# Optimization experiments

Hardware: AMD Instinct MI355X
Metric: run time of the kernel (lower is better)

## Reference

```python
import jax, jax.numpy as jnp
import numpy as np

G, NPG, HID, NLAYERS, MAXZ, K = 256, 128, 256, 3, 1000, 30
N = G * NPG          # 32768 nodes
E = N * 16           # 524288 edges
TOTAL_DIM = HID * NLAYERS + 1  # 769


def setup_inputs():
    key = jax.random.key(0)
    ks = jax.random.split(key, 12)
    z = jax.random.randint(ks[0], (N,), 0, MAXZ)
    edge_index = jax.random.randint(ks[1], (2, E), 0, N)
    batch = jnp.arange(N) // NPG  # contiguous equal-size graphs
    emb = jax.random.normal(ks[2], (MAXZ, HID), jnp.float32)
    s = 1.0 / np.sqrt(HID)
    gcn_w = jax.random.normal(ks[3], (NLAYERS, HID, HID), jnp.float32) * s
    gcn_b = jnp.zeros((NLAYERS, HID), jnp.float32)
    gcn_w_last = jax.random.normal(ks[4], (HID, 1), jnp.float32) * s
    gcn_b_last = jnp.zeros((1,), jnp.float32)
    conv1_w = jax.random.normal(ks[5], (16, 1, 5), jnp.float32) * (1.0 / np.sqrt(5))
    conv1_b = jnp.zeros((16,), jnp.float32)
    conv2_w = jax.random.normal(ks[6], (32, 16, 5), jnp.float32) * (1.0 / np.sqrt(80))
    conv2_b = jnp.zeros((32,), jnp.float32)
    kd = K * TOTAL_DIM            # 23070
    flat = 32 * ((kd - 4) // 2 - 4)  # 368928
    lin1_w = jax.random.normal(ks[7], (128, flat), jnp.float32) * (1.0 / np.sqrt(flat))
    lin1_b = jnp.zeros((128,), jnp.float32)
    lin2_w = jax.random.normal(ks[8], (1, 128), jnp.float32) * (1.0 / np.sqrt(128))
    lin2_b = jnp.zeros((1,), jnp.float32)
    return dict(z=z, edge_index=edge_index, batch=batch, emb=emb, gcn_w=gcn_w,
                gcn_b=gcn_b, gcn_w_last=gcn_w_last, gcn_b_last=gcn_b_last,
                conv1_w=conv1_w, conv1_b=conv1_b, conv2_w=conv2_w, conv2_b=conv2_b,
                lin1_w=lin1_w, lin1_b=lin1_b, lin2_w=lin2_w, lin2_b=lin2_b)


def reference(z, edge_index, batch, emb, gcn_w, gcn_b, gcn_w_last, gcn_b_last,
              conv1_w, conv1_b, conv2_w, conv2_b, lin1_w, lin1_b, lin2_w, lin2_b):
    src, dst = edge_index[0], edge_index[1]
    # GCNConv normalization with self-loops: D^{-1/2}(A+I)D^{-1/2}
    deg = 1.0 + jax.ops.segment_sum(jnp.ones((E,), jnp.float32), dst, num_segments=N)
    dinv = jax.lax.rsqrt(deg)
    enorm = dinv[src] * dinv[dst]   # per-edge norm
    snorm = 1.0 / deg               # self-loop norm

    def gcn(x, W, b):
        xw = x @ W
        agg = jax.ops.segment_sum(enorm[:, None] * xw[src], dst, num_segments=N)
        return agg + snorm[:, None] * xw + b

    x = emb[z]
    xs = []
    for i in range(NLAYERS):
        x = jnp.tanh(gcn(x, gcn_w[i], gcn_b[i]))
        xs.append(x)
    xs.append(jnp.tanh(gcn(x, gcn_w_last, gcn_b_last)))
    h = jnp.concatenate(xs, axis=-1)  # [N, TOTAL_DIM]

    # global_sort_pool: per-graph descending sort by last channel, keep top-k
    hg = h.reshape(G, NPG, TOTAL_DIM)
    order = jnp.argsort(-hg[:, :, -1], axis=1)
    hg = jnp.take_along_axis(hg, order[:, :, None], axis=1)[:, :K]
    p = hg.reshape(G, 1, K * TOTAL_DIM)

    dn = ('NCH', 'OIH', 'NCH')
    c = jax.lax.conv_general_dilated(p, conv1_w, (1,), 'VALID', dimension_numbers=dn)
    c = jax.nn.relu(c + conv1_b[None, :, None])
    c = jax.lax.reduce_window(c, -jnp.inf, jax.lax.max, (1, 1, 2), (1, 1, 2), 'VALID')
    c = jax.lax.conv_general_dilated(c, conv2_w, (1,), 'VALID', dimension_numbers=dn)
    c = jax.nn.relu(c + conv2_b[None, :, None])
    f = c.reshape(G, -1)
    f = jax.nn.relu(f @ lin1_w.T + lin1_b)
    return (f @ lin2_w.T + lin2_b).reshape(-1)
```

## Files before the change

kernel.cpp:

```cpp
#include <hip/hip_runtime.h>

#define NN      32768
#define EE      524288
#define GG      256
#define NPG     128
#define HID     256
#define KTOP    30
#define TD      769
#define HSTR    772
#define PLEN    23070
#define C1LEN   23066
#define POOLLEN 11533
#define C2LEN   11529
#define FLAT    368928
#define L1_KRANGE 1920
#define L1_KS   193

__global__ __launch_bounds__(256) void k_deg(const int* __restrict__ dst, int* __restrict__ deg_cnt) {
    int e = blockIdx.x * 256 + threadIdx.x;
    atomicAdd(&deg_cnt[dst[e]], 1);
}

__global__ __launch_bounds__(256) void k_norm(const int* __restrict__ deg_cnt,
                                              float* __restrict__ dinv, float* __restrict__ snorm) {
    int n = blockIdx.x * 256 + threadIdx.x;
    float dg = 1.0f + (float)deg_cnt[n];
    dinv[n] = rsqrtf(dg);
    snorm[n] = 1.0f / dg;
}

__global__ __launch_bounds__(1024) void k_scan(const int* __restrict__ deg_cnt, int* __restrict__ row_start) {
    __shared__ int sA[1024];
    int t = threadIdx.x;
    int base = t * 32;
    int s = 0;
    for (int i = 0; i < 32; i++) s += deg_cnt[base + i];
    sA[t] = s;
    __syncthreads();
    for (int off = 1; off < 1024; off <<= 1) {
        int v = (t >= off) ? sA[t - off] : 0;
        __syncthreads();
        sA[t] += v;
        __syncthreads();
    }
    int run = sA[t] - s;
    for (int i = 0; i < 32; i++) { row_start[base + i] = run; run += deg_cnt[base + i]; }
}

__global__ __launch_bounds__(256) void k_csrfill(const int* __restrict__ src, const int* __restrict__ dst,
                                                 const int* __restrict__ row_start, int* __restrict__ fill,
                                                 const float* __restrict__ dinv,
                                                 int* __restrict__ csr_src, float* __restrict__ csr_w) {
    int e = blockIdx.x * 256 + threadIdx.x;
    int s = src[e], d = dst[e];
    int pos = row_start[d] + atomicAdd(&fill[d], 1);
    csr_src[pos] = s;
    csr_w[pos] = dinv[s] * dinv[d];
}

__global__ __launch_bounds__(256) void k_embed(const int* __restrict__ z, const float* __restrict__ emb,
                                               float* __restrict__ x) {
    int i = blockIdx.x * 256 + threadIdx.x;
    int n = i >> 6, l = i & 63;
    ((float4*)x)[(size_t)n * 64 + l] = ((const float4*)emb)[(size_t)z[n] * 64 + l];
}

__global__ __launch_bounds__(256) void k_gemm_gcn(const float* __restrict__ A, const float* __restrict__ B,
                                                  float* __restrict__ C) {
    __shared__ float As[16][132];
    __shared__ float Bs[16][132];
    int m0 = blockIdx.x * 128;
    int n0 = blockIdx.y * 128;
    int tid = threadIdx.x;
    int ty = tid >> 4, tx = tid & 15;
    float acc[8][8] = {};
    for (int k0 = 0; k0 < 256; k0 += 16) {
        {
            int m = tid >> 2, kq = (tid & 3) * 4;
            #pragma unroll
            for (int r = 0; r < 2; r++) {
                float4 v = *(const float4*)&A[(size_t)(m0 + m + 64 * r) * 256 + k0 + kq];
                As[kq + 0][m + 64 * r] = v.x;
                As[kq + 1][m + 64 * r] = v.y;
                As[kq + 2][m + 64 * r] = v.z;
                As[kq + 3][m + 64 * r] = v.w;
            }
            int n = (tid & 31) * 4, kk = tid >> 5;
            #pragma unroll
            for (int r = 0; r < 2; r++) {
                float4 v = *(const float4*)&B[(size_t)(k0 + kk + 8 * r) * 256 + n0 + n];
                *(float4*)&Bs[kk + 8 * r][n] = v;
            }
        }
        __syncthreads();
        #pragma unroll
        for (int k = 0; k < 16; k++) {
            float a[8], b[8];
            *(float4*)&a[0] = *(float4*)&As[k][ty * 8];
            *(float4*)&a[4] = *(float4*)&As[k][ty * 8 + 4];
            *(float4*)&b[0] = *(float4*)&Bs[k][tx * 8];
            *(float4*)&b[4] = *(float4*)&Bs[k][tx * 8 + 4];
            #pragma unroll
            for (int i = 0; i < 8; i++)
                #pragma unroll
                for (int j = 0; j < 8; j++) acc[i][j] += a[i] * b[j];
        }
        __syncthreads();
    }
    #pragma unroll
    for (int i = 0; i < 8; i++) {
        int m = m0 + ty * 8 + i;
        float4 v0 = make_float4(acc[i][0], acc[i][1], acc[i][2], acc[i][3]);
        float4 v1 = make_float4(acc[i][4], acc[i][5], acc[i][6], acc[i][7]);
        *(float4*)&C[(size_t)m * 256 + n0 + tx * 8] = v0;
        *(float4*)&C[(size_t)m * 256 + n0 + tx * 8 + 4] = v1;
    }
}

__global__ __launch_bounds__(256) void k_agg(const float* __restrict__ xw, const int* __restrict__ row_start,
                                             const int* __restrict__ deg_cnt, const int* __restrict__ csr_src,
                                             const float* __restrict__ csr_w, const float* __restrict__ snorm,
                                             const float* __restrict__ bias, float* __restrict__ xn,
                                             float* __restrict__ h, int hoff) {
    int d = blockIdx.x * 4 + (threadIdx.x >> 6);
    int l = threadIdx.x & 63;
    float4 v = ((const float4*)xw)[(size_t)d * 64 + l];
    float sn = snorm[d];
    float4 acc = make_float4(sn * v.x, sn * v.y, sn * v.z, sn * v.w);
    int st = row_start[d], cnt = deg_cnt[d];
    for (int j = 0; j < cnt; j++) {
        int s = csr_src[st + j];
        float w = csr_w[st + j];
        float4 u = ((const float4*)xw)[(size_t)s * 64 + l];
        acc.x += w * u.x; acc.y += w * u.y; acc.z += w * u.z; acc.w += w * u.w;
    }
    float4 b = ((const float4*)bias)[l];
    acc.x = tanhf(acc.x + b.x);
    acc.y = tanhf(acc.y + b.y);
    acc.z = tanhf(acc.z + b.z);
    acc.w = tanhf(acc.w + b.w);
    ((float4*)xn)[(size_t)d * 64 + l] = acc;
    *(float4*)&h[(size_t)d * HSTR + hoff + l * 4] = acc;
}

__global__ __launch_bounds__(256) void k_dot_last(const float* __restrict__ x, const float* __restrict__ wl,
                                                  float* __restrict__ xwl) {
    int d = blockIdx.x * 4 + (threadIdx.x >> 6);
    int l = threadIdx.x & 63;
    float4 v = ((const float4*)x)[(size_t)d * 64 + l];
    float4 w = ((const float4*)wl)[l];
    float s = v.x * w.x + v.y * w.y + v.z * w.z + v.w * w.w;
    #pragma unroll
    for (int off = 32; off; off >>= 1) s += __shfl_down(s, off, 64);
    if (l == 0) xwl[d] = s;
}

__global__ __launch_bounds__(256) void k_agg_last(const float* __restrict__ xwl, const int* __restrict__ row_start,
                                                  const int* __restrict__ deg_cnt, const int* __restrict__ csr_src,
                                                  const float* __restrict__ csr_w, const float* __restrict__ snorm,
                                                  const float* __restrict__ blast, float* __restrict__ h) {
    int d = blockIdx.x * 256 + threadIdx.x;
    float acc = snorm[d] * xwl[d];
    int st = row_start[d], cnt = deg_cnt[d];
    for (int j = 0; j < cnt; j++) acc += csr_w[st + j] * xwl[csr_src[st + j]];
    h[(size_t)d * HSTR + 768] = tanhf(acc + blast[0]);
}

__global__ __launch_bounds__(128) void k_sort_gather(const float* __restrict__ h, float* __restrict__ P) {
    __shared__ float kk[128];
    __shared__ int ii[128];
    int g = blockIdx.x, t = threadIdx.x;
    kk[t] = h[(size_t)(g * 128 + t) * HSTR + 768];
    ii[t] = t;
    __syncthreads();
    for (int size = 2; size <= 128; size <<= 1) {
        for (int stride = size >> 1; stride > 0; stride >>= 1) {
            int p = t ^ stride;
            if (p > t) {
                float ka = kk[t], kbv = kk[p];
                int ia = ii[t], ib = ii[p];
                bool aFirst = (ka > kbv) || (ka == kbv && ia < ib);
                bool asc = (t & size) == 0;
                if (asc != aFirst) { kk[t] = kbv; kk[p] = ka; ii[t] = ib; ii[p] = ia; }
            }
            __syncthreads();
        }
    }
    float* Pg = P + (size_t)g * PLEN;
    for (int r = 0; r < KTOP; r++) {
        const float* srcp = h + (size_t)(g * 128 + ii[r]) * HSTR;
        for (int c = t; c < TD; c += 128) Pg[(size_t)r * TD + c] = srcp[c];
    }
}

#define JT 128
__global__ __launch_bounds__(256) void k_conv(const float* __restrict__ P,
                                              const float* __restrict__ w1, const float* __restrict__ b1,
                                              const float* __restrict__ w2, const float* __restrict__ b2,
                                              float* __restrict__ f) {
    __shared__ float sl[272];
    __shared__ float pool[16][136];
    __shared__ float w2t[80][32];
    __shared__ float w1s[16][5];
    __shared__ float b1s[16];
    __shared__ float b2s[32];
    int g = blockIdx.x;
    int j0 = blockIdx.y * JT;
    int tid = threadIdx.x;
    const float* Pg = P + (size_t)g * PLEN;
    for (int i = tid; i < 268; i += 256) sl[i] = Pg[min(2 * j0 + i, PLEN - 1)];
    for (int i = tid; i < 80; i += 256) w1s[i / 5][i % 5] = w1[i];
    if (tid < 16) b1s[tid] = b1[tid];
    if (tid < 32) b2s[tid] = b2[tid];
    for (int i = tid; i < 2560; i += 256) {
        int c2 = i / 80, rem = i % 80;
        w2t[rem][c2] = w2[i];
    }
    __syncthreads();
    for (int i = tid; i < 16 * 132; i += 256) {
        int c1 = i / 132, t = i % 132;
        int u = 2 * t;
        float a = b1s[c1], b = a;
        #pragma unroll
        for (int q = 0; q < 5; q++) {
            a += w1s[c1][q] * sl[u + q];
            b += w1s[c1][q] * sl[u + 1 + q];
        }
        pool[c1][t] = fmaxf(fmaxf(a, b), 0.0f);
    }
    __syncthreads();
    int wv = tid >> 6;
    int jl = tid & 63;
    int c2o = wv * 8;
    float acc[8][2];
    #pragma unroll
    for (int cc = 0; cc < 8; cc++) {
        float bb = b2s[c2o + cc];
        acc[cc][0] = bb; acc[cc][1] = bb;
    }
    #pragma unroll 4
    for (int c1 = 0; c1 < 16; c1++) {
        #pragma unroll
        for (int k = 0; k < 5; k++) {
            float4 w0 = *(float4*)&w2t[c1 * 5 + k][c2o];
            float4 w1v = *(float4*)&w2t[c1 * 5 + k][c2o + 4];
            float p0 = pool[c1][jl + k];
            float p1 = pool[c1][jl + 64 + k];
            acc[0][0] += w0.x * p0; acc[0][1] += w0.x * p1;
            acc[1][0] += w0.y * p0; acc[1][1] += w0.y * p1;
            acc[2][0] += w0.z * p0; acc[2][1] += w0.z * p1;
            acc[3][0] += w0.w * p0; acc[3][1] += w0.w * p1;
            acc[4][0] += w1v.x * p0; acc[4][1] += w1v.x * p1;
            acc[5][0] += w1v.y * p0; acc[5][1] += w1v.y * p1;
            acc[6][0] += w1v.z * p0; acc[6][1] += w1v.z * p1;
            acc[7][0] += w1v.w * p0; acc[7][1] += w1v.w * p1;
        }
    }
    size_t fg = (size_t)g * FLAT;
    #pragma unroll
    for (int cc = 0; cc < 8; cc++) {
        #pragma unroll
        for (int jj = 0; jj < 2; jj++) {
            int j = j0 + jl + 64 * jj;
            if (j < C2LEN) f[fg + (size_t)(c2o + cc) * C2LEN + j] = fmaxf(acc[cc][jj], 0.0f);
        }
    }
}

__global__ __launch_bounds__(256) void k_lin1(const float* __restrict__ f, const float* __restrict__ W,
                                              float* __restrict__ partial) {
    __shared__ float As[32][68];
    __shared__ float Bs[32][132];
    int m0 = blockIdx.x * 64;
    int ks = blockIdx.y;
    int kbase = ks * L1_KRANGE;
    int kend = min(kbase + L1_KRANGE, FLAT);
    int tid = threadIdx.x;
    int ty = tid >> 5, tx = tid & 31;
    float acc[8][4] = {};
    for (int k0 = kbase; k0 < kend; k0 += 32) {
        {
            int m = tid >> 2, kq = (tid & 3) * 8;
            #pragma unroll
            for (int r = 0; r < 2; r++) {
                int k = kq + r * 4;
                float4 v = *(const float4*)&f[(size_t)(m0 + m) * FLAT + k0 + k];
                As[k + 0][m] = v.x; As[k + 1][m] = v.y; As[k + 2][m] = v.z; As[k + 3][m] = v.w;
            }
            int n = tid >> 3, kq2 = (tid & 7) * 4;
            #pragma unroll
            for (int r = 0; r < 4; r++) {
                int nn = n + 32 * r;
                float4 v = *(const float4*)&W[(size_t)nn * FLAT + k0 + kq2];
                Bs[kq2 + 0][nn] = v.x; Bs[kq2 + 1][nn] = v.y; Bs[kq2 + 2][nn] = v.z; Bs[kq2 + 3][nn] = v.w;
            }
        }
        __syncthreads();
        #pragma unroll
        for (int k = 0; k < 32; k++) {
            float a[8], bv[4];
            *(float4*)&a[0] = *(float4*)&As[k][ty * 8];
            *(float4*)&a[4] = *(float4*)&As[k][ty * 8 + 4];
            *(float4*)&bv[0] = *(float4*)&Bs[k][tx * 4];
            #pragma unroll
            for (int i = 0; i < 8; i++)
                #pragma unroll
                for (int j = 0; j < 4; j++) acc[i][j] += a[i] * bv[j];
        }
        __syncthreads();
    }
    #pragma unroll
    for (int i = 0; i < 8; i++) {
        int m = m0 + ty * 8 + i;
        float4 v = make_float4(acc[i][0], acc[i][1], acc[i][2], acc[i][3]);
        *(float4*)&partial[((size_t)ks * 256 + m) * 128 + tx * 4] = v;
    }
}

__global__ __launch_bounds__(128) void k_reduce(const float* __restrict__ partial, const float* __restrict__ lb1,
                                                const float* __restrict__ lw2, const float* __restrict__ lb2,
                                                float* __restrict__ out) {
    int g = blockIdx.x, o = threadIdx.x;
    float s = 0.0f;
    for (int ks = 0; ks < L1_KS; ks++) s += partial[((size_t)ks * 256 + g) * 128 + o];
    float v = fmaxf(s + lb1[o], 0.0f) * lw2[o];
    #pragma unroll
    for (int off = 32; off; off >>= 1) v += __shfl_down(v, off, 64);
    __shared__ float red[2];
    if ((threadIdx.x & 63) == 0) red[threadIdx.x >> 6] = v;
    __syncthreads();
    if (threadIdx.x == 0) out[g] = red[0] + red[1] + lb2[0];
}

extern "C" void kernel_launch(void* const* d_in, const int* in_sizes, int n_in,
                              void* d_out, int out_size, void* d_ws, size_t ws_size,
                              hipStream_t stream) {
    const int*   z     = (const int*)d_in[0];
    const int*   ei    = (const int*)d_in[1];
    const int*   srcv  = ei;
    const int*   dstv  = ei + EE;
    const float* emb   = (const float*)d_in[3];
    const float* gcnw  = (const float*)d_in[4];
    const float* gcnb  = (const float*)d_in[5];
    const float* wlast = (const float*)d_in[6];
    const float* blast = (const float*)d_in[7];
    const float* w1    = (const float*)d_in[8];
    const float* b1    = (const float*)d_in[9];
    const float* w2    = (const float*)d_in[10];
    const float* b2    = (const float*)d_in[11];
    const float* l1w   = (const float*)d_in[12];
    const float* l1b   = (const float*)d_in[13];
    const float* l2w   = (const float*)d_in[14];
    const float* l2b   = (const float*)d_in[15];
    float* out = (float*)d_out;

    char* base = (char*)d_ws;
    const size_t FB = ((size_t)GG * FLAT * 4 + 511) & ~(size_t)511;
    float* fbuf = (float*)base;
    char* p = base;
    auto alloc = [&](size_t bytes) { void* r = (void*)p; p += (bytes + 511) & ~(size_t)511; return r; };
    int*   deg_cnt = (int*)  alloc((size_t)NN * 4);
    int*   fill    = (int*)  alloc((size_t)NN * 4);
    int*   rowst   = (int*)  alloc((size_t)NN * 4);
    int*   csr_src = (int*)  alloc((size_t)EE * 4);
    float* csr_w   = (float*)alloc((size_t)EE * 4);
    float* dinv    = (float*)alloc((size_t)NN * 4);
    float* snorm   = (float*)alloc((size_t)NN * 4);
    float* xA      = (float*)alloc((size_t)NN * 256 * 4);
    float* xB      = (float*)alloc((size_t)NN * 256 * 4);
    float* xw      = (float*)alloc((size_t)NN * 256 * 4);
    float* h       = (float*)alloc((size_t)NN * HSTR * 4);
    float* xwl     = (float*)alloc((size_t)NN * 4);
    float* P       = (float*)(base + FB);
    float* partial = (float*)(base + FB + (((size_t)GG * PLEN * 4 + 511) & ~(size_t)511));
    (void)ws_size; (void)in_sizes; (void)n_in; (void)out_size;

    hipMemsetAsync(deg_cnt, 0, (size_t)NN * 4, stream);
    hipMemsetAsync(fill,    0, (size_t)NN * 4, stream);

    k_deg    <<<EE / 256, 256, 0, stream>>>(dstv, deg_cnt);
    k_norm   <<<NN / 256, 256, 0, stream>>>(deg_cnt, dinv, snorm);
    k_scan   <<<1, 1024, 0, stream>>>(deg_cnt, rowst);
    k_csrfill<<<EE / 256, 256, 0, stream>>>(srcv, dstv, rowst, fill, dinv, csr_src, csr_w);
    k_embed  <<<NN * 64 / 256, 256, 0, stream>>>(z, emb, xA);

    float* xc = xA;
    float* xn = xB;
    for (int layer = 0; layer < 3; layer++) {
        k_gemm_gcn<<<dim3(NN / 128, 2), 256, 0, stream>>>(xc, gcnw + (size_t)layer * 65536, xw);
        k_agg<<<NN / 4, 256, 0, stream>>>(xw, rowst, deg_cnt, csr_src, csr_w, snorm,
                                          gcnb + layer * 256, xn, h, layer * 256);
        float* t = xc; xc = xn; xn = t;
    }
    k_dot_last<<<NN / 4, 256, 0, stream>>>(xc, wlast, xwl);
    k_agg_last<<<NN / 256, 256, 0, stream>>>(xwl, rowst, deg_cnt, csr_src, csr_w, snorm, blast, h);

    k_sort_gather<<<GG, 128, 0, stream>>>(h, P);

    k_conv<<<dim3(GG, (C2LEN + JT - 1) / JT), 256, 0, stream>>>(P, w1, b1, w2, b2, fbuf);

    k_lin1  <<<dim3(4, L1_KS), 256, 0, stream>>>(fbuf, l1w, partial);
    k_reduce<<<GG, 128, 0, stream>>>(partial, l1b, l2w, l2b, out);
}
```

Baseline: 1.477 ms.

## Retile lin1 GEMM, fuse last-layer dot into aggregation, split conv1 input even/odd

The lin1 split-K GEMM now uses 128x128 output tiles with an 8x8 per-thread microtile, a 16-deep k step and a smaller k range per block. This halves the number of times the large lin1 weight matrix is re-read across M tiles and raises the block count along K. The separate k_dot_last kernel is folded into the third k_agg launch, which saves one pass over the node features and one launch. The conv1 input in shared memory is split into even and odd arrays, so the stride-2 pooled convolution reads consecutive addresses. The trade-off is more partial sums for k_reduce to add and higher register use in lin1.

```diff
diff --git a/kernel.cpp b/kernel.cpp
--- a/kernel.cpp
+++ b/kernel.cpp
@@ -13,8 +13,8 @@
 #define POOLLEN 11533
 #define C2LEN   11529
 #define FLAT    368928
-#define L1_KRANGE 1920
-#define L1_KS   193
+#define L1_KRANGE 1024
+#define L1_KS   361
 
 __global__ __launch_bounds__(256) void k_deg(const int* __restrict__ dst, int* __restrict__ deg_cnt) {
     int e = blockIdx.x * 256 + threadIdx.x;
@@ -121,7 +121,8 @@
                                              const int* __restrict__ deg_cnt, const int* __restrict__ csr_src,
                                              const float* __restrict__ csr_w, const float* __restrict__ snorm,
                                              const float* __restrict__ bias, float* __restrict__ xn,
-                                             float* __restrict__ h, int hoff) {
+                                             float* __restrict__ h, int hoff,
+                                             const float* __restrict__ wl, float* __restrict__ xwl) {
     int d = blockIdx.x * 4 + (threadIdx.x >> 6);
     int l = threadIdx.x & 63;
     float4 v = ((const float4*)xw)[(size_t)d * 64 + l];
@@ -141,18 +142,13 @@
     acc.w = tanhf(acc.w + b.w);
     ((float4*)xn)[(size_t)d * 64 + l] = acc;
     *(float4*)&h[(size_t)d * HSTR + hoff + l * 4] = acc;
-}
-
-__global__ __launch_bounds__(256) void k_dot_last(const float* __restrict__ x, const float* __restrict__ wl,
-                                                  float* __restrict__ xwl) {
-    int d = blockIdx.x * 4 + (threadIdx.x >> 6);
-    int l = threadIdx.x & 63;
-    float4 v = ((const float4*)x)[(size_t)d * 64 + l];
-    float4 w = ((const float4*)wl)[l];
-    float s = v.x * w.x + v.y * w.y + v.z * w.z + v.w * w.w;
-    #pragma unroll
-    for (int off = 32; off; off >>= 1) s += __shfl_down(s, off, 64);
-    if (l == 0) xwl[d] = s;
+    if (wl != nullptr) {
+        float4 w4 = ((const float4*)wl)[l];
+        float s = acc.x * w4.x + acc.y * w4.y + acc.z * w4.z + acc.w * w4.w;
+        #pragma unroll
+        for (int off = 32; off; off >>= 1) s += __shfl_down(s, off, 64);
+        if (l == 0) xwl[d] = s;
+    }
 }
 
 __global__ __launch_bounds__(256) void k_agg_last(const float* __restrict__ xwl, const int* __restrict__ row_start,
@@ -198,7 +194,8 @@
                                               const float* __restrict__ w1, const float* __restrict__ b1,
                                               const float* __restrict__ w2, const float* __restrict__ b2,
                                               float* __restrict__ f) {
-    __shared__ float sl[272];
+    __shared__ float sle[136];
+    __shared__ float slo[136];
     __shared__ float pool[16][136];
     __shared__ float w2t[80][32];
     __shared__ float w1s[16][5];
@@ -208,7 +205,10 @@
     int j0 = blockIdx.y * JT;
     int tid = threadIdx.x;
     const float* Pg = P + (size_t)g * PLEN;
-    for (int i = tid; i < 268; i += 256) sl[i] = Pg[min(2 * j0 + i, PLEN - 1)];
+    for (int i = tid; i < 268; i += 256) {
+        float v = Pg[min(2 * j0 + i, PLEN - 1)];
+        if (i & 1) slo[i >> 1] = v; else sle[i >> 1] = v;
+    }
     for (int i = tid; i < 80; i += 256) w1s[i / 5][i % 5] = w1[i];
     if (tid < 16) b1s[tid] = b1[tid];
     if (tid < 32) b2s[tid] = b2[tid];
@@ -219,13 +219,10 @@
     __syncthreads();
     for (int i = tid; i < 16 * 132; i += 256) {
         int c1 = i / 132, t = i % 132;
-        int u = 2 * t;
-        float a = b1s[c1], b = a;
-        #pragma unroll
-        for (int q = 0; q < 5; q++) {
-            a += w1s[c1][q] * sl[u + q];
-            b += w1s[c1][q] * sl[u + 1 + q];
-        }
+        float e0 = sle[t], o0 = slo[t], e1 = sle[t + 1], o1 = slo[t + 1], e2 = sle[t + 2], o2 = slo[t + 2];
+        float w0 = w1s[c1][0], w1v = w1s[c1][1], w2v = w1s[c1][2], w3 = w1s[c1][3], w4 = w1s[c1][4];
+        float a = b1s[c1] + w0 * e0 + w1v * o0 + w2v * e1 + w3 * o1 + w4 * e2;
+        float b = b1s[c1] + w0 * o0 + w1v * e1 + w2v * o1 + w3 * e2 + w4 * o2;
         pool[c1][t] = fmaxf(fmaxf(a, b), 0.0f);
     }
     __syncthreads();
@@ -269,51 +266,56 @@
 
 __global__ __launch_bounds__(256) void k_lin1(const float* __restrict__ f, const float* __restrict__ W,
                                               float* __restrict__ partial) {
-    __shared__ float As[32][68];
-    __shared__ float Bs[32][132];
-    int m0 = blockIdx.x * 64;
+    __shared__ float As[16][132];
+    __shared__ float Bs[16][132];
+    int m0 = blockIdx.x * 128;
     int ks = blockIdx.y;
     int kbase = ks * L1_KRANGE;
     int kend = min(kbase + L1_KRANGE, FLAT);
     int tid = threadIdx.x;
-    int ty = tid >> 5, tx = tid & 31;
-    float acc[8][4] = {};
-    for (int k0 = kbase; k0 < kend; k0 += 32) {
+    int ty = tid >> 4, tx = tid & 15;
+    float acc[8][8] = {};
+    for (int k0 = kbase; k0 < kend; k0 += 16) {
         {
-            int m = tid >> 2, kq = (tid & 3) * 8;
+            int m = tid >> 2, kq = (tid & 3) * 4;
             #pragma unroll
             for (int r = 0; r < 2; r++) {
-                int k = kq + r * 4;
-                float4 v = *(const float4*)&f[(size_t)(m0 + m) * FLAT + k0 + k];
-                As[k + 0][m] = v.x; As[k + 1][m] = v.y; As[k + 2][m] = v.z; As[k + 3][m] = v.w;
+                float4 v = *(const float4*)&f[(size_t)(m0 + m + 64 * r) * FLAT + k0 + kq];
+                As[kq + 0][m + 64 * r] = v.x;
+                As[kq + 1][m + 64 * r] = v.y;
+                As[kq + 2][m + 64 * r] = v.z;
+                As[kq + 3][m + 64 * r] = v.w;
             }
-            int n = tid >> 3, kq2 = (tid & 7) * 4;
-            #pragma unroll
-            for (int r = 0; r < 4; r++) {
-                int nn = n + 32 * r;
-                float4 v = *(const float4*)&W[(size_t)nn * FLAT + k0 + kq2];
-                Bs[kq2 + 0][nn] = v.x; Bs[kq2 + 1][nn] = v.y; Bs[kq2 + 2][nn] = v.z; Bs[kq2 + 3][nn] = v.w;
+            int n = tid >> 1, kq2 = (tid & 1) * 8;
+            #pragma unroll
+            for (int r = 0; r < 2; r++) {
+                int k = kq2 + r * 4;
+                float4 v = *(const float4*)&W[(size_t)n * FLAT + k0 + k];
+                Bs[k + 0][n] = v.x; Bs[k + 1][n] = v.y; Bs[k + 2][n] = v.z; Bs[k + 3][n] = v.w;
             }
         }
         __syncthreads();
         #pragma unroll
-        for (int k = 0; k < 32; k++) {
-            float a[8], bv[4];
+        for (int k = 0; k < 16; k++) {
+            float a[8], b[8];
             *(float4*)&a[0] = *(float4*)&As[k][ty * 8];
             *(float4*)&a[4] = *(float4*)&As[k][ty * 8 + 4];
-            *(float4*)&bv[0] = *(float4*)&Bs[k][tx * 4];
+            *(float4*)&b[0] = *(float4*)&Bs[k][tx * 8];
+            *(float4*)&b[4] = *(float4*)&Bs[k][tx * 8 + 4];
             #pragma unroll
             for (int i = 0; i < 8; i++)
                 #pragma unroll
-                for (int j = 0; j < 4; j++) acc[i][j] += a[i] * bv[j];
+                for (int j = 0; j < 8; j++) acc[i][j] += a[i] * b[j];
         }
         __syncthreads();
     }
     #pragma unroll
     for (int i = 0; i < 8; i++) {
         int m = m0 + ty * 8 + i;
-        float4 v = make_float4(acc[i][0], acc[i][1], acc[i][2], acc[i][3]);
-        *(float4*)&partial[((size_t)ks * 256 + m) * 128 + tx * 4] = v;
+        float4 v0 = make_float4(acc[i][0], acc[i][1], acc[i][2], acc[i][3]);
+        float4 v1 = make_float4(acc[i][4], acc[i][5], acc[i][6], acc[i][7]);
+        *(float4*)&partial[((size_t)ks * 256 + m) * 128 + tx * 8] = v0;
+        *(float4*)&partial[((size_t)ks * 256 + m) * 128 + tx * 8 + 4] = v1;
     }
 }
 
@@ -388,17 +390,17 @@
     float* xn = xB;
     for (int layer = 0; layer < 3; layer++) {
         k_gemm_gcn<<<dim3(NN / 128, 2), 256, 0, stream>>>(xc, gcnw + (size_t)layer * 65536, xw);
+        const float* wl = (layer == 2) ? wlast : nullptr;
         k_agg<<<NN / 4, 256, 0, stream>>>(xw, rowst, deg_cnt, csr_src, csr_w, snorm,
-                                          gcnb + layer * 256, xn, h, layer * 256);
+                                          gcnb + layer * 256, xn, h, layer * 256, wl, xwl);
         float* t = xc; xc = xn; xn = t;
     }
-    k_dot_last<<<NN / 4, 256, 0, stream>>>(xc, wlast, xwl);
     k_agg_last<<<NN / 256, 256, 0, stream>>>(xwl, rowst, deg_cnt, csr_src, csr_w, snorm, blast, h);
 
     k_sort_gather<<<GG, 128, 0, stream>>>(h, P);
 
     k_conv<<<dim3(GG, (C2LEN + JT - 1) / JT), 256, 0, stream>>>(P, w1, b1, w2, b2, fbuf);
 
-    k_lin1  <<<dim3(4, L1_KS), 256, 0, stream>>>(fbuf, l1w, partial);
+    k_lin1  <<<dim3(2, L1_KS), 256, 0, stream>>>(fbuf, l1w, partial);
     k_reduce<<<GG, 128, 0, stream>>>(partial, l1b, l2w, l2b, out);
 }
```

New measurement: 1.454 ms. Within noise of the previous version (-1.5%).
